# Optimization experiments

Hardware: AMD Instinct MI355X
Metric: run time of the kernel (lower is better)

The kernel has to match this reference:

```python
import jax, jax.numpy as jnp
import numpy as np

LR = 0.001       # ISTA step size (default in _IstaStep)
GAMMA = 0.1      # lambdav sparsity penalty (gamma init kwarg)
N_STEPS = 10     # number of unrolled ISTA iterations


def _soft_threshold(x, t):
    # _proxOp: max(x - t, 0) + min(x + t, 0)
    return jnp.maximum(x - t, 0.0) + jnp.minimum(x + t, 0.0)


def setup_inputs() -> dict:
    key = jax.random.key(0)
    k1, k2 = jax.random.split(key)
    B, I, O = 131072, 128, 256
    inputs = jax.random.normal(k1, (B, I), dtype=jnp.float32)
    # glorot_uniform for W of shape (output_dim, input_dim)
    scale = float(np.sqrt(6.0 / (O + I)))
    W = jax.random.uniform(k2, (O, I), dtype=jnp.float32, minval=-scale, maxval=scale)
    return {"inputs": inputs, "W": W}


def reference(inputs, W):
    # inputs: [B, I]; W: [O, I]; states x: [B, O]
    B = inputs.shape[0]
    O = W.shape[0]
    x0 = jnp.zeros((B, O), dtype=inputs.dtype)

    def step(x, _):
        recon = x @ W                              # [B, I], linear activation
        # analytic grad of sum((inputs - recon)^2) w.r.t. x (what T.grad computes)
        grad = 2.0 * (recon - inputs) @ W.T        # [B, O]
        new_x = _soft_threshold(x - LR * grad, LR * GAMMA)
        # theano.gradient.disconnected_grad on the new state each step
        new_x = jax.lax.stop_gradient(new_x)
        return new_x, None

    x_final, _ = jax.lax.scan(step, x0, None, length=N_STEPS)
    # return_reconstruction=True -> dot(outs, W)
    return x_final @ W
```

## Files before the change

kernel.cpp:

```cpp
#include <hip/hip_runtime.h>
#include <hip/hip_bf16.h>

typedef __attribute__((ext_vector_type(4))) float  f32x4;
typedef __attribute__((ext_vector_type(16))) float f32x16;
typedef __attribute__((ext_vector_type(8))) short  s16x8;
typedef __attribute__((ext_vector_type(4))) short  s16x4;

#define THR_  1.0e-4f
#define SC_   2.0e-3f

__device__ __forceinline__ unsigned short f2bf(float f) {
  union { __hip_bfloat16 b; unsigned short u; } cv;
  cv.b = __float2bfloat16(f);
  return cv.u;
}

__device__ __forceinline__ float sthr(float v) {
  return v - fmaxf(fminf(v, THR_), -THR_);
}

__global__ void sc_prep(const float* __restrict__ W, unsigned short* __restrict__ ws) {
  const int b = blockIdx.x;
  const int l = threadIdx.x;
  const int r = l & 31, h = l >> 5;
  if (b < 128) {
    const int kc = b >> 3, ntg = b & 7;
    const int n = ntg * 32 + r;
    const int k0 = kc * 16 + 8 * h;
    float s[8];
    #pragma unroll
    for (int j = 0; j < 8; ++j) s[j] = 0.0f;
    for (int i = 0; i < 128; ++i) {
      const float wn = W[n * 128 + i];
      #pragma unroll
      for (int j = 0; j < 8; ++j) s[j] += W[(k0 + j) * 128 + i] * wn;
    }
    unsigned short* dst = ws + ((unsigned)b * 64u + l) * 8u;
    #pragma unroll
    for (int j = 0; j < 8; ++j) dst[j] = f2bf(-SC_ * s[j]);
  } else if (b < 192) {
    const int bb = b - 128;
    const int kc = bb >> 3, ntg = bb & 7;
    const int n = ntg * 32 + r;
    const int k0 = kc * 16 + 8 * h;
    unsigned short* dst = ws + 65536u + ((unsigned)bb * 64u + l) * 8u;
    #pragma unroll
    for (int j = 0; j < 8; ++j) dst[j] = f2bf(SC_ * W[n * 128 + k0 + j]);
  } else {
    const int bb = b - 192;
    const int kc = bb >> 2, it = bb & 3;
    const int i = it * 32 + r;
    const int n0 = kc * 16 + 8 * h;
    unsigned short* dst = ws + 98304u + ((unsigned)bb * 64u + l) * 8u;
    #pragma unroll
    for (int j = 0; j < 8; ++j) dst[j] = f2bf(W[(n0 + j) * 128 + i]);
  }
}

__global__ __launch_bounds__(256, 2) void sc_fused(
    const float* __restrict__ inp,
    const unsigned short* __restrict__ wsp,
    float* __restrict__ outp)
{
  __shared__ __align__(16) unsigned char lds[33280];

  const int tid = threadIdx.x;
  const int l = tid & 63;
  const int w = tid >> 6;
  const int h = l >> 5;
  const int r31 = l & 31;
  const long row0 = (long)blockIdx.x * 32;

  const int rB0 = r31 * 520 + h * 16;
  const int rB1 = rB0 + 16640;
  const int wB0 = r31 * 520 + h * 8 + w * 128;
  const int wB1 = wB0 + 16640;

  #pragma unroll
  for (int rep = 0; rep < 4; ++rep) {
    const int flat = rep * 256 + tid;
    const int rr = flat >> 5;
    const int c4 = flat & 31;
    const f32x4 v = *reinterpret_cast<const f32x4*>(inp + (row0 + rr) * 128 + c4 * 4);
    s16x4 p;
    p[0] = (short)f2bf(v[0]); p[1] = (short)f2bf(v[1]);
    p[2] = (short)f2bf(v[2]); p[3] = (short)f2bf(v[3]);
    *reinterpret_cast<s16x4*>(lds + 16640 + rr * 264 + c4 * 8) = p;
  }

  s16x8 gfr[32];
  #pragma unroll
  for (int kc = 0; kc < 8; ++kc)
    #pragma unroll
    for (int nt = 0; nt < 2; ++nt)
      gfr[kc * 2 + nt] = *reinterpret_cast<const s16x8*>(
          wsp + 65536u + ((unsigned)(kc * 8 + w * 2 + nt) * 64u + l) * 8u);

  __syncthreads();

  f32x16 xacc[2], creg[2];
  #pragma unroll
  for (int nt = 0; nt < 2; ++nt)
    #pragma unroll
    for (int e = 0; e < 16; ++e) xacc[nt][e] = 0.0f;

  const int ib = 16640 + r31 * 264 + h * 16;
  #pragma unroll
  for (int kc = 0; kc < 8; ++kc) {
    const s16x8 b = *reinterpret_cast<const s16x8*>(lds + ib + kc * 32);
    __builtin_amdgcn_s_setprio(1);
    #pragma unroll
    for (int nt = 0; nt < 2; ++nt)
      xacc[nt] = __builtin_amdgcn_mfma_f32_32x32x16_bf16(gfr[kc * 2 + nt], b, xacc[nt], 0, 0, 0);
    __builtin_amdgcn_s_setprio(0);
  }

  #pragma unroll
  for (int nt = 0; nt < 2; ++nt) {
    creg[nt] = xacc[nt];
    #pragma unroll
    for (int q = 0; q < 4; ++q) {
      float f0 = sthr(xacc[nt][4 * q + 0]), f1 = sthr(xacc[nt][4 * q + 1]);
      float f2 = sthr(xacc[nt][4 * q + 2]), f3 = sthr(xacc[nt][4 * q + 3]);
      xacc[nt][4 * q + 0] = f0; xacc[nt][4 * q + 1] = f1;
      xacc[nt][4 * q + 2] = f2; xacc[nt][4 * q + 3] = f3;
      s16x4 p;
      p[0] = (short)f2bf(f0); p[1] = (short)f2bf(f1);
      p[2] = (short)f2bf(f2); p[3] = (short)f2bf(f3);
      *reinterpret_cast<s16x4*>(lds + wB0 + nt * 64 + q * 16) = p;
    }
  }

  #pragma unroll
  for (int kc = 0; kc < 16; ++kc)
    #pragma unroll
    for (int nt = 0; nt < 2; ++nt)
      gfr[kc * 2 + nt] = *reinterpret_cast<const s16x8*>(
          wsp + ((unsigned)(kc * 8 + w * 2 + nt) * 64u + l) * 8u);

  auto STEP = [&](const int rb, const int wb) {
    __syncthreads();
    #pragma unroll
    for (int nt = 0; nt < 2; ++nt)
      #pragma unroll
      for (int e = 0; e < 16; ++e) xacc[nt][e] += creg[nt][e];
    #pragma unroll
    for (int kc = 0; kc < 16; ++kc) {
      const s16x8 b = *reinterpret_cast<const s16x8*>(lds + rb + kc * 32);
      __builtin_amdgcn_s_setprio(1);
      #pragma unroll
      for (int nt = 0; nt < 2; ++nt)
        xacc[nt] = __builtin_amdgcn_mfma_f32_32x32x16_bf16(gfr[kc * 2 + nt], b, xacc[nt], 0, 0, 0);
      __builtin_amdgcn_s_setprio(0);
    }
    #pragma unroll
    for (int nt = 0; nt < 2; ++nt)
      #pragma unroll
      for (int q = 0; q < 4; ++q) {
        float f0 = sthr(xacc[nt][4 * q + 0]), f1 = sthr(xacc[nt][4 * q + 1]);
        float f2 = sthr(xacc[nt][4 * q + 2]), f3 = sthr(xacc[nt][4 * q + 3]);
        xacc[nt][4 * q + 0] = f0; xacc[nt][4 * q + 1] = f1;
        xacc[nt][4 * q + 2] = f2; xacc[nt][4 * q + 3] = f3;
        s16x4 p;
        p[0] = (short)f2bf(f0); p[1] = (short)f2bf(f1);
        p[2] = (short)f2bf(f2); p[3] = (short)f2bf(f3);
        *reinterpret_cast<s16x4*>(lds + wb + nt * 64 + q * 16) = p;
      }
  };

  #pragma unroll 1
  for (int p = 0; p < 4; ++p) {
    STEP(rB0, wB1);
    STEP(rB1, wB0);
  }
  STEP(rB0, wB1);

  __syncthreads();
  #pragma unroll
  for (int kc = 0; kc < 16; ++kc)
    gfr[kc] = *reinterpret_cast<const s16x8*>(
        wsp + 98304u + ((unsigned)(kc * 4 + w) * 64u + l) * 8u);
  f32x16 oacc;
  #pragma unroll
  for (int e = 0; e < 16; ++e) oacc[e] = 0.0f;
  #pragma unroll
  for (int kc = 0; kc < 16; ++kc) {
    const s16x8 b = *reinterpret_cast<const s16x8*>(lds + rB1 + kc * 32);
    __builtin_amdgcn_s_setprio(1);
    oacc = __builtin_amdgcn_mfma_f32_32x32x16_bf16(gfr[kc], b, oacc, 0, 0, 0);
    __builtin_amdgcn_s_setprio(0);
  }
  const int ob = r31 * 520 + h * 16 + w * 128;
  #pragma unroll
  for (int q = 0; q < 4; ++q) {
    f32x4 p;
    p[0] = oacc[4 * q + 0]; p[1] = oacc[4 * q + 1];
    p[2] = oacc[4 * q + 2]; p[3] = oacc[4 * q + 3];
    *reinterpret_cast<f32x4*>(lds + ob + q * 32) = p;
  }
  __syncthreads();
  #pragma unroll
  for (int rep = 0; rep < 4; ++rep) {
    const int flat = rep * 256 + tid;
    const int rr = flat >> 5;
    const int c4 = flat & 31;
    const f32x4 v = *reinterpret_cast<const f32x4*>(lds + rr * 520 + c4 * 16);
    *reinterpret_cast<f32x4*>(outp + (row0 + rr) * 128 + c4 * 4) = v;
  }
}

extern "C" void kernel_launch(void* const* d_in, const int* in_sizes, int n_in,
                              void* d_out, int out_size, void* d_ws, size_t ws_size,
                              hipStream_t stream) {
  const float* inp = (const float*)d_in[0];
  const float* W   = (const float*)d_in[1];
  unsigned short* ws = (unsigned short*)d_ws;
  float* outp = (float*)d_out;
  const int B = in_sizes[0] / 128;
  sc_prep<<<256, 64, 0, stream>>>(W, ws);
  sc_fused<<<B / 32, 256, 0, stream>>>(inp, ws, outp);
}
```

Baseline: 184.6 us.

## Split MFMA accumulators into two chains and stagger alternate block groups

```diff
diff --git a/kernel.cpp b/kernel.cpp
--- a/kernel.cpp
+++ b/kernel.cpp
@@ -64,6 +64,11 @@
 {
   __shared__ __align__(16) unsigned char lds[33280];
 
+  if ((blockIdx.x >> 8) & 1) {
+    __builtin_amdgcn_s_sleep(15);
+    __builtin_amdgcn_s_sleep(5);
+  }
+
   const int tid = threadIdx.x;
   const int l = tid & 63;
   const int w = tid >> 6;
@@ -98,38 +103,49 @@
 
   __syncthreads();
 
-  f32x16 xacc[2], creg[2];
+  f32x16 accA[2], accB[2], creg[2];
   #pragma unroll
   for (int nt = 0; nt < 2; ++nt)
     #pragma unroll
-    for (int e = 0; e < 16; ++e) xacc[nt][e] = 0.0f;
+    for (int e = 0; e < 16; ++e) { accA[nt][e] = 0.0f; accB[nt][e] = 0.0f; }
 
   const int ib = 16640 + r31 * 264 + h * 16;
   #pragma unroll
-  for (int kc = 0; kc < 8; ++kc) {
-    const s16x8 b = *reinterpret_cast<const s16x8*>(lds + ib + kc * 32);
+  for (int kc = 0; kc < 4; ++kc) {
+    const s16x8 bA = *reinterpret_cast<const s16x8*>(lds + ib + kc * 32);
+    const s16x8 bB = *reinterpret_cast<const s16x8*>(lds + ib + (kc + 4) * 32);
     __builtin_amdgcn_s_setprio(1);
     #pragma unroll
     for (int nt = 0; nt < 2; ++nt)
-      xacc[nt] = __builtin_amdgcn_mfma_f32_32x32x16_bf16(gfr[kc * 2 + nt], b, xacc[nt], 0, 0, 0);
+      accA[nt] = __builtin_amdgcn_mfma_f32_32x32x16_bf16(gfr[kc * 2 + nt], bA, accA[nt], 0, 0, 0);
+    #pragma unroll
+    for (int nt = 0; nt < 2; ++nt)
+      accB[nt] = __builtin_amdgcn_mfma_f32_32x32x16_bf16(gfr[(kc + 4) * 2 + nt], bB, accB[nt], 0, 0, 0);
     __builtin_amdgcn_s_setprio(0);
   }
 
   #pragma unroll
-  for (int nt = 0; nt < 2; ++nt) {
-    creg[nt] = xacc[nt];
+  for (int nt = 0; nt < 2; ++nt)
     #pragma unroll
     for (int q = 0; q < 4; ++q) {
-      float f0 = sthr(xacc[nt][4 * q + 0]), f1 = sthr(xacc[nt][4 * q + 1]);
-      float f2 = sthr(xacc[nt][4 * q + 2]), f3 = sthr(xacc[nt][4 * q + 3]);
-      xacc[nt][4 * q + 0] = f0; xacc[nt][4 * q + 1] = f1;
-      xacc[nt][4 * q + 2] = f2; xacc[nt][4 * q + 3] = f3;
+      float f0 = accA[nt][4 * q + 0] + accB[nt][4 * q + 0];
+      float f1 = accA[nt][4 * q + 1] + accB[nt][4 * q + 1];
+      float f2 = accA[nt][4 * q + 2] + accB[nt][4 * q + 2];
+      float f3 = accA[nt][4 * q + 3] + accB[nt][4 * q + 3];
+      creg[nt][4 * q + 0] = f0; creg[nt][4 * q + 1] = f1;
+      creg[nt][4 * q + 2] = f2; creg[nt][4 * q + 3] = f3;
+      f0 = sthr(f0); f1 = sthr(f1); f2 = sthr(f2); f3 = sthr(f3);
       s16x4 p;
       p[0] = (short)f2bf(f0); p[1] = (short)f2bf(f1);
       p[2] = (short)f2bf(f2); p[3] = (short)f2bf(f3);
       *reinterpret_cast<s16x4*>(lds + wB0 + nt * 64 + q * 16) = p;
+      accA[nt][4 * q + 0] = f0 + creg[nt][4 * q + 0];
+      accA[nt][4 * q + 1] = f1 + creg[nt][4 * q + 1];
+      accA[nt][4 * q + 2] = f2 + creg[nt][4 * q + 2];
+      accA[nt][4 * q + 3] = f3 + creg[nt][4 * q + 3];
+      accB[nt][4 * q + 0] = 0.0f; accB[nt][4 * q + 1] = 0.0f;
+      accB[nt][4 * q + 2] = 0.0f; accB[nt][4 * q + 3] = 0.0f;
     }
-  }
 
   #pragma unroll
   for (int kc = 0; kc < 16; ++kc)
@@ -141,30 +157,36 @@
   auto STEP = [&](const int rb, const int wb) {
     __syncthreads();
     #pragma unroll
-    for (int nt = 0; nt < 2; ++nt)
-      #pragma unroll
-      for (int e = 0; e < 16; ++e) xacc[nt][e] += creg[nt][e];
-    #pragma unroll
-    for (int kc = 0; kc < 16; ++kc) {
-      const s16x8 b = *reinterpret_cast<const s16x8*>(lds + rb + kc * 32);
+    for (int kc = 0; kc < 8; ++kc) {
+      const s16x8 bA = *reinterpret_cast<const s16x8*>(lds + rb + kc * 32);
+      const s16x8 bB = *reinterpret_cast<const s16x8*>(lds + rb + (kc + 8) * 32);
       __builtin_amdgcn_s_setprio(1);
       #pragma unroll
       for (int nt = 0; nt < 2; ++nt)
-        xacc[nt] = __builtin_amdgcn_mfma_f32_32x32x16_bf16(gfr[kc * 2 + nt], b, xacc[nt], 0, 0, 0);
+        accA[nt] = __builtin_amdgcn_mfma_f32_32x32x16_bf16(gfr[kc * 2 + nt], bA, accA[nt], 0, 0, 0);
+      #pragma unroll
+      for (int nt = 0; nt < 2; ++nt)
+        accB[nt] = __builtin_amdgcn_mfma_f32_32x32x16_bf16(gfr[(kc + 8) * 2 + nt], bB, accB[nt], 0, 0, 0);
       __builtin_amdgcn_s_setprio(0);
     }
     #pragma unroll
     for (int nt = 0; nt < 2; ++nt)
       #pragma unroll
       for (int q = 0; q < 4; ++q) {
-        float f0 = sthr(xacc[nt][4 * q + 0]), f1 = sthr(xacc[nt][4 * q + 1]);
-        float f2 = sthr(xacc[nt][4 * q + 2]), f3 = sthr(xacc[nt][4 * q + 3]);
-        xacc[nt][4 * q + 0] = f0; xacc[nt][4 * q + 1] = f1;
-        xacc[nt][4 * q + 2] = f2; xacc[nt][4 * q + 3] = f3;
+        float f0 = sthr(accA[nt][4 * q + 0] + accB[nt][4 * q + 0]);
+        float f1 = sthr(accA[nt][4 * q + 1] + accB[nt][4 * q + 1]);
+        float f2 = sthr(accA[nt][4 * q + 2] + accB[nt][4 * q + 2]);
+        float f3 = sthr(accA[nt][4 * q + 3] + accB[nt][4 * q + 3]);
         s16x4 p;
         p[0] = (short)f2bf(f0); p[1] = (short)f2bf(f1);
         p[2] = (short)f2bf(f2); p[3] = (short)f2bf(f3);
         *reinterpret_cast<s16x4*>(lds + wb + nt * 64 + q * 16) = p;
+        accA[nt][4 * q + 0] = f0 + creg[nt][4 * q + 0];
+        accA[nt][4 * q + 1] = f1 + creg[nt][4 * q + 1];
+        accA[nt][4 * q + 2] = f2 + creg[nt][4 * q + 2];
+        accA[nt][4 * q + 3] = f3 + creg[nt][4 * q + 3];
+        accB[nt][4 * q + 0] = 0.0f; accB[nt][4 * q + 1] = 0.0f;
+        accB[nt][4 * q + 2] = 0.0f; accB[nt][4 * q + 3] = 0.0f;
       }
   };
 
@@ -180,22 +202,24 @@
   for (int kc = 0; kc < 16; ++kc)
     gfr[kc] = *reinterpret_cast<const s16x8*>(
         wsp + 98304u + ((unsigned)(kc * 4 + w) * 64u + l) * 8u);
-  f32x16 oacc;
-  #pragma unroll
-  for (int e = 0; e < 16; ++e) oacc[e] = 0.0f;
-  #pragma unroll
-  for (int kc = 0; kc < 16; ++kc) {
-    const s16x8 b = *reinterpret_cast<const s16x8*>(lds + rB1 + kc * 32);
+  f32x16 oA, oB;
+  #pragma unroll
+  for (int e = 0; e < 16; ++e) { oA[e] = 0.0f; oB[e] = 0.0f; }
+  #pragma unroll
+  for (int kc = 0; kc < 8; ++kc) {
+    const s16x8 bA = *reinterpret_cast<const s16x8*>(lds + rB1 + kc * 32);
+    const s16x8 bB = *reinterpret_cast<const s16x8*>(lds + rB1 + (kc + 8) * 32);
     __builtin_amdgcn_s_setprio(1);
-    oacc = __builtin_amdgcn_mfma_f32_32x32x16_bf16(gfr[kc], b, oacc, 0, 0, 0);
+    oA = __builtin_amdgcn_mfma_f32_32x32x16_bf16(gfr[kc], bA, oA, 0, 0, 0);
+    oB = __builtin_amdgcn_mfma_f32_32x32x16_bf16(gfr[kc + 8], bB, oB, 0, 0, 0);
     __builtin_amdgcn_s_setprio(0);
   }
   const int ob = r31 * 520 + h * 16 + w * 128;
   #pragma unroll
   for (int q = 0; q < 4; ++q) {
     f32x4 p;
-    p[0] = oacc[4 * q + 0]; p[1] = oacc[4 * q + 1];
-    p[2] = oacc[4 * q + 2]; p[3] = oacc[4 * q + 3];
+    p[0] = oA[4 * q + 0] + oB[4 * q + 0]; p[1] = oA[4 * q + 1] + oB[4 * q + 1];
+    p[2] = oA[4 * q + 2] + oB[4 * q + 2]; p[3] = oA[4 * q + 3] + oB[4 * q + 3];
     *reinterpret_cast<f32x4*>(lds + ob + q * 32) = p;
   }
   __syncthreads();
```

Result: faster. 179.7 us (-2.7%).

## Process two row tiles per block and interleave their ISTA steps

Applied to the files above, without the earlier changes.

```diff
diff --git a/kernel.cpp b/kernel.cpp
--- a/kernel.cpp
+++ b/kernel.cpp
@@ -14,9 +14,14 @@
   cv.b = __float2bfloat16(f);
   return cv.u;
 }
-
 __device__ __forceinline__ float sthr(float v) {
   return v - fmaxf(fminf(v, THR_), -THR_);
+}
+__device__ __forceinline__ float bflo(unsigned u) {
+  return __builtin_bit_cast(float, u << 16);
+}
+__device__ __forceinline__ float bfhi(unsigned u) {
+  return __builtin_bit_cast(float, u & 0xffff0000u);
 }
 
 __global__ void sc_prep(const float* __restrict__ W, unsigned short* __restrict__ ws) {
@@ -62,22 +67,26 @@
     const unsigned short* __restrict__ wsp,
     float* __restrict__ outp)
 {
-  __shared__ __align__(16) unsigned char lds[33280];
+  __shared__ __align__(16) unsigned char lds[66560];
+
+  if ((blockIdx.x >> 8) & 1) {
+    __builtin_amdgcn_s_sleep(15);
+    __builtin_amdgcn_s_sleep(5);
+  }
 
   const int tid = threadIdx.x;
   const int l = tid & 63;
   const int w = tid >> 6;
   const int h = l >> 5;
   const int r31 = l & 31;
-  const long row0 = (long)blockIdx.x * 32;
-
-  const int rB0 = r31 * 520 + h * 16;
-  const int rB1 = rB0 + 16640;
-  const int wB0 = r31 * 520 + h * 8 + w * 128;
-  const int wB1 = wB0 + 16640;
-
-  #pragma unroll
-  for (int rep = 0; rep < 4; ++rep) {
+  const long row0 = (long)blockIdx.x * 64;
+
+  const int rB = r31 * 520 + h * 16;
+  const int wB = r31 * 520 + h * 8 + w * 128;
+  const int ob = r31 * 520 + w * 128 + h * 16;
+
+  #pragma unroll
+  for (int rep = 0; rep < 8; ++rep) {
     const int flat = rep * 256 + tid;
     const int rr = flat >> 5;
     const int c4 = flat & 31;
@@ -85,7 +94,8 @@
     s16x4 p;
     p[0] = (short)f2bf(v[0]); p[1] = (short)f2bf(v[1]);
     p[2] = (short)f2bf(v[2]); p[3] = (short)f2bf(v[3]);
-    *reinterpret_cast<s16x4*>(lds + 16640 + rr * 264 + c4 * 8) = p;
+    const int base = 16640 + (rr >> 5) * 33280 + (rr & 31) * 264;
+    *reinterpret_cast<s16x4*>(lds + base + c4 * 8) = p;
   }
 
   s16x8 gfr[32];
@@ -98,38 +108,51 @@
 
   __syncthreads();
 
-  f32x16 xacc[2], creg[2];
-  #pragma unroll
-  for (int nt = 0; nt < 2; ++nt)
-    #pragma unroll
-    for (int e = 0; e < 16; ++e) xacc[nt][e] = 0.0f;
-
-  const int ib = 16640 + r31 * 264 + h * 16;
+  f32x16 accT[2], accU[2];
+  #pragma unroll
+  for (int nt = 0; nt < 2; ++nt)
+    #pragma unroll
+    for (int e = 0; e < 16; ++e) { accT[nt][e] = 0.0f; accU[nt][e] = 0.0f; }
+
+  const int ibT = 16640 + r31 * 264 + h * 16;
+  const int ibU = ibT + 33280;
   #pragma unroll
   for (int kc = 0; kc < 8; ++kc) {
-    const s16x8 b = *reinterpret_cast<const s16x8*>(lds + ib + kc * 32);
+    const s16x8 bT = *reinterpret_cast<const s16x8*>(lds + ibT + kc * 32);
+    const s16x8 bU = *reinterpret_cast<const s16x8*>(lds + ibU + kc * 32);
     __builtin_amdgcn_s_setprio(1);
-    #pragma unroll
-    for (int nt = 0; nt < 2; ++nt)
-      xacc[nt] = __builtin_amdgcn_mfma_f32_32x32x16_bf16(gfr[kc * 2 + nt], b, xacc[nt], 0, 0, 0);
+    accT[0] = __builtin_amdgcn_mfma_f32_32x32x16_bf16(gfr[kc * 2 + 0], bT, accT[0], 0, 0, 0);
+    accT[1] = __builtin_amdgcn_mfma_f32_32x32x16_bf16(gfr[kc * 2 + 1], bT, accT[1], 0, 0, 0);
+    accU[0] = __builtin_amdgcn_mfma_f32_32x32x16_bf16(gfr[kc * 2 + 0], bU, accU[0], 0, 0, 0);
+    accU[1] = __builtin_amdgcn_mfma_f32_32x32x16_bf16(gfr[kc * 2 + 1], bU, accU[1], 0, 0, 0);
     __builtin_amdgcn_s_setprio(0);
   }
 
-  #pragma unroll
-  for (int nt = 0; nt < 2; ++nt) {
-    creg[nt] = xacc[nt];
+  unsigned cpT[16], cpU[16];
+  #pragma unroll
+  for (int nt = 0; nt < 2; ++nt)
+    #pragma unroll
+    for (int j = 0; j < 8; ++j) {
+      cpT[nt * 8 + j] = (unsigned)f2bf(accT[nt][2 * j]) |
+                        ((unsigned)f2bf(accT[nt][2 * j + 1]) << 16);
+      cpU[nt * 8 + j] = (unsigned)f2bf(accU[nt][2 * j]) |
+                        ((unsigned)f2bf(accU[nt][2 * j + 1]) << 16);
+    }
+
+  #pragma unroll
+  for (int nt = 0; nt < 2; ++nt)
     #pragma unroll
     for (int q = 0; q < 4; ++q) {
-      float f0 = sthr(xacc[nt][4 * q + 0]), f1 = sthr(xacc[nt][4 * q + 1]);
-      float f2 = sthr(xacc[nt][4 * q + 2]), f3 = sthr(xacc[nt][4 * q + 3]);
-      xacc[nt][4 * q + 0] = f0; xacc[nt][4 * q + 1] = f1;
-      xacc[nt][4 * q + 2] = f2; xacc[nt][4 * q + 3] = f3;
+      float x0 = sthr(accT[nt][4 * q + 0]), x1 = sthr(accT[nt][4 * q + 1]);
+      float x2 = sthr(accT[nt][4 * q + 2]), x3 = sthr(accT[nt][4 * q + 3]);
       s16x4 p;
-      p[0] = (short)f2bf(f0); p[1] = (short)f2bf(f1);
-      p[2] = (short)f2bf(f2); p[3] = (short)f2bf(f3);
-      *reinterpret_cast<s16x4*>(lds + wB0 + nt * 64 + q * 16) = p;
-    }
-  }
+      p[0] = (short)f2bf(x0); p[1] = (short)f2bf(x1);
+      p[2] = (short)f2bf(x2); p[3] = (short)f2bf(x3);
+      *reinterpret_cast<s16x4*>(lds + 0 + wB + nt * 64 + q * 16) = p;
+      const unsigned pa = cpT[nt * 8 + q * 2], pb = cpT[nt * 8 + q * 2 + 1];
+      accT[nt][4 * q + 0] = x0 + bflo(pa); accT[nt][4 * q + 1] = x1 + bfhi(pa);
+      accT[nt][4 * q + 2] = x2 + bflo(pb); accT[nt][4 * q + 3] = x3 + bfhi(pb);
+    }
 
   #pragma unroll
   for (int kc = 0; kc < 16; ++kc)
@@ -138,73 +161,101 @@
       gfr[kc * 2 + nt] = *reinterpret_cast<const s16x8*>(
           wsp + ((unsigned)(kc * 8 + w * 2 + nt) * 64u + l) * 8u);
 
-  auto STEP = [&](const int rb, const int wb) {
-    __syncthreads();
-    #pragma unroll
-    for (int nt = 0; nt < 2; ++nt)
-      #pragma unroll
-      for (int e = 0; e < 16; ++e) xacc[nt][e] += creg[nt][e];
+  auto MSTEP = [&](f32x16* acc, const int rbase) {
+    __builtin_amdgcn_s_setprio(1);
     #pragma unroll
     for (int kc = 0; kc < 16; ++kc) {
-      const s16x8 b = *reinterpret_cast<const s16x8*>(lds + rb + kc * 32);
-      __builtin_amdgcn_s_setprio(1);
-      #pragma unroll
-      for (int nt = 0; nt < 2; ++nt)
-        xacc[nt] = __builtin_amdgcn_mfma_f32_32x32x16_bf16(gfr[kc * 2 + nt], b, xacc[nt], 0, 0, 0);
-      __builtin_amdgcn_s_setprio(0);
-    }
+      const s16x8 b = *reinterpret_cast<const s16x8*>(lds + rbase + rB + kc * 32);
+      acc[0] = __builtin_amdgcn_mfma_f32_32x32x16_bf16(gfr[kc * 2 + 0], b, acc[0], 0, 0, 0);
+      acc[1] = __builtin_amdgcn_mfma_f32_32x32x16_bf16(gfr[kc * 2 + 1], b, acc[1], 0, 0, 0);
+    }
+    __builtin_amdgcn_s_setprio(0);
+  };
+  auto WB = [&](f32x16* acc, const unsigned* cp, const int wbase) {
     #pragma unroll
     for (int nt = 0; nt < 2; ++nt)
       #pragma unroll
       for (int q = 0; q < 4; ++q) {
-        float f0 = sthr(xacc[nt][4 * q + 0]), f1 = sthr(xacc[nt][4 * q + 1]);
-        float f2 = sthr(xacc[nt][4 * q + 2]), f3 = sthr(xacc[nt][4 * q + 3]);
-        xacc[nt][4 * q + 0] = f0; xacc[nt][4 * q + 1] = f1;
-        xacc[nt][4 * q + 2] = f2; xacc[nt][4 * q + 3] = f3;
+        float x0 = sthr(acc[nt][4 * q + 0]), x1 = sthr(acc[nt][4 * q + 1]);
+        float x2 = sthr(acc[nt][4 * q + 2]), x3 = sthr(acc[nt][4 * q + 3]);
         s16x4 p;
-        p[0] = (short)f2bf(f0); p[1] = (short)f2bf(f1);
-        p[2] = (short)f2bf(f2); p[3] = (short)f2bf(f3);
-        *reinterpret_cast<s16x4*>(lds + wb + nt * 64 + q * 16) = p;
+        p[0] = (short)f2bf(x0); p[1] = (short)f2bf(x1);
+        p[2] = (short)f2bf(x2); p[3] = (short)f2bf(x3);
+        *reinterpret_cast<s16x4*>(lds + wbase + wB + nt * 64 + q * 16) = p;
+        const unsigned pa = cp[nt * 8 + q * 2], pb = cp[nt * 8 + q * 2 + 1];
+        acc[nt][4 * q + 0] = x0 + bflo(pa); acc[nt][4 * q + 1] = x1 + bfhi(pa);
+        acc[nt][4 * q + 2] = x2 + bflo(pb); acc[nt][4 * q + 3] = x3 + bfhi(pb);
       }
   };
 
+  __syncthreads();
+
   #pragma unroll 1
-  for (int p = 0; p < 4; ++p) {
-    STEP(rB0, wB1);
-    STEP(rB1, wB0);
-  }
-  STEP(rB0, wB1);
-
-  __syncthreads();
+  for (int i = 0; i < 9; ++i) {
+    const int par = i & 1;
+    MSTEP(accT, par ? 16640 : 0);
+    WB(accU, cpU, par ? 49920 : 33280);
+    __syncthreads();
+    MSTEP(accU, par ? 49920 : 33280);
+    WB(accT, cpT, par ? 0 : 16640);
+    __syncthreads();
+  }
+
   #pragma unroll
   for (int kc = 0; kc < 16; ++kc)
     gfr[kc] = *reinterpret_cast<const s16x8*>(
         wsp + 98304u + ((unsigned)(kc * 4 + w) * 64u + l) * 8u);
-  f32x16 oacc;
-  #pragma unroll
-  for (int e = 0; e < 16; ++e) oacc[e] = 0.0f;
+
+  #pragma unroll
+  for (int e = 0; e < 16; ++e) accT[0][e] = 0.0f;
+  __builtin_amdgcn_s_setprio(1);
   #pragma unroll
   for (int kc = 0; kc < 16; ++kc) {
-    const s16x8 b = *reinterpret_cast<const s16x8*>(lds + rB1 + kc * 32);
-    __builtin_amdgcn_s_setprio(1);
-    oacc = __builtin_amdgcn_mfma_f32_32x32x16_bf16(gfr[kc], b, oacc, 0, 0, 0);
-    __builtin_amdgcn_s_setprio(0);
-  }
-  const int ob = r31 * 520 + h * 16 + w * 128;
+    const s16x8 b = *reinterpret_cast<const s16x8*>(lds + 16640 + rB + kc * 32);
+    accT[0] = __builtin_amdgcn_mfma_f32_32x32x16_bf16(gfr[kc], b, accT[0], 0, 0, 0);
+  }
+  __builtin_amdgcn_s_setprio(0);
+  #pragma unroll
+  for (int nt = 0; nt < 2; ++nt)
+    #pragma unroll
+    for (int q = 0; q < 4; ++q) {
+      float x0 = sthr(accU[nt][4 * q + 0]), x1 = sthr(accU[nt][4 * q + 1]);
+      float x2 = sthr(accU[nt][4 * q + 2]), x3 = sthr(accU[nt][4 * q + 3]);
+      s16x4 p;
+      p[0] = (short)f2bf(x0); p[1] = (short)f2bf(x1);
+      p[2] = (short)f2bf(x2); p[3] = (short)f2bf(x3);
+      *reinterpret_cast<s16x4*>(lds + 49920 + wB + nt * 64 + q * 16) = p;
+    }
+  __syncthreads();
+
+  #pragma unroll
+  for (int e = 0; e < 16; ++e) accU[0][e] = 0.0f;
+  __builtin_amdgcn_s_setprio(1);
+  #pragma unroll
+  for (int kc = 0; kc < 16; ++kc) {
+    const s16x8 b = *reinterpret_cast<const s16x8*>(lds + 49920 + rB + kc * 32);
+    accU[0] = __builtin_amdgcn_mfma_f32_32x32x16_bf16(gfr[kc], b, accU[0], 0, 0, 0);
+  }
+  __builtin_amdgcn_s_setprio(0);
   #pragma unroll
   for (int q = 0; q < 4; ++q) {
-    f32x4 p;
-    p[0] = oacc[4 * q + 0]; p[1] = oacc[4 * q + 1];
-    p[2] = oacc[4 * q + 2]; p[3] = oacc[4 * q + 3];
-    *reinterpret_cast<f32x4*>(lds + ob + q * 32) = p;
-  }
-  __syncthreads();
-  #pragma unroll
-  for (int rep = 0; rep < 4; ++rep) {
+    f32x4 pT, pU;
+    pT[0] = accT[0][4 * q + 0]; pT[1] = accT[0][4 * q + 1];
+    pT[2] = accT[0][4 * q + 2]; pT[3] = accT[0][4 * q + 3];
+    pU[0] = accU[0][4 * q + 0]; pU[1] = accU[0][4 * q + 1];
+    pU[2] = accU[0][4 * q + 2]; pU[3] = accU[0][4 * q + 3];
+    *reinterpret_cast<f32x4*>(lds + 0     + ob + q * 32) = pT;
+    *reinterpret_cast<f32x4*>(lds + 33280 + ob + q * 32) = pU;
+  }
+  __syncthreads();
+
+  #pragma unroll
+  for (int rep = 0; rep < 8; ++rep) {
     const int flat = rep * 256 + tid;
     const int rr = flat >> 5;
     const int c4 = flat & 31;
-    const f32x4 v = *reinterpret_cast<const f32x4*>(lds + rr * 520 + c4 * 16);
+    const int base = (rr >> 5) * 33280 + (rr & 31) * 520;
+    const f32x4 v = *reinterpret_cast<const f32x4*>(lds + base + c4 * 16);
     *reinterpret_cast<f32x4*>(outp + (row0 + rr) * 128 + c4 * 4) = v;
   }
 }
@@ -218,5 +269,5 @@
   float* outp = (float*)d_out;
   const int B = in_sizes[0] / 128;
   sc_prep<<<256, 64, 0, stream>>>(W, ws);
-  sc_fused<<<B / 32, 256, 0, stream>>>(inp, ws, outp);
-}
+  sc_fused<<<B / 64, 256, 0, stream>>>(inp, ws, outp);
+}
```

Measured after the change: 234.1 us. 1.27x slower.

## Process 64 rows per block and pack the constant term as bf16

Applied to the files above, without the earlier changes.

```diff
diff --git a/kernel.cpp b/kernel.cpp
--- a/kernel.cpp
+++ b/kernel.cpp
@@ -14,9 +14,14 @@
   cv.b = __float2bfloat16(f);
   return cv.u;
 }
-
 __device__ __forceinline__ float sthr(float v) {
   return v - fmaxf(fminf(v, THR_), -THR_);
+}
+__device__ __forceinline__ float bflo(unsigned u) {
+  return __builtin_bit_cast(float, u << 16);
+}
+__device__ __forceinline__ float bfhi(unsigned u) {
+  return __builtin_bit_cast(float, u & 0xffff0000u);
 }
 
 __global__ void sc_prep(const float* __restrict__ W, unsigned short* __restrict__ ws) {
@@ -62,22 +67,22 @@
     const unsigned short* __restrict__ wsp,
     float* __restrict__ outp)
 {
-  __shared__ __align__(16) unsigned char lds[33280];
+  __shared__ __align__(16) unsigned char lds[66560];
 
   const int tid = threadIdx.x;
   const int l = tid & 63;
   const int w = tid >> 6;
   const int h = l >> 5;
   const int r31 = l & 31;
-  const long row0 = (long)blockIdx.x * 32;
-
-  const int rB0 = r31 * 520 + h * 16;
-  const int rB1 = rB0 + 16640;
-  const int wB0 = r31 * 520 + h * 8 + w * 128;
-  const int wB1 = wB0 + 16640;
-
-  #pragma unroll
-  for (int rep = 0; rep < 4; ++rep) {
+  const long row0 = (long)blockIdx.x * 64;
+
+  const int rBm0 = r31 * 520 + h * 16;
+  const int rBm1 = rBm0 + 32 * 520;
+  const int wBm0 = r31 * 520 + w * 128 + h * 8;
+  const int wBm1 = wBm0 + 32 * 520;
+
+  #pragma unroll
+  for (int rep = 0; rep < 8; ++rep) {
     const int flat = rep * 256 + tid;
     const int rr = flat >> 5;
     const int c4 = flat & 31;
@@ -85,7 +90,7 @@
     s16x4 p;
     p[0] = (short)f2bf(v[0]); p[1] = (short)f2bf(v[1]);
     p[2] = (short)f2bf(v[2]); p[3] = (short)f2bf(v[3]);
-    *reinterpret_cast<s16x4*>(lds + 16640 + rr * 264 + c4 * 8) = p;
+    *reinterpret_cast<s16x4*>(lds + 33280 + rr * 264 + c4 * 8) = p;
   }
 
   s16x8 gfr[32];
@@ -98,38 +103,58 @@
 
   __syncthreads();
 
-  f32x16 xacc[2], creg[2];
+  f32x16 acc[2][2];
   #pragma unroll
   for (int nt = 0; nt < 2; ++nt)
     #pragma unroll
-    for (int e = 0; e < 16; ++e) xacc[nt][e] = 0.0f;
-
-  const int ib = 16640 + r31 * 264 + h * 16;
+    for (int mg = 0; mg < 2; ++mg)
+      #pragma unroll
+      for (int e = 0; e < 16; ++e) acc[nt][mg][e] = 0.0f;
+
+  const int ib0 = 33280 + r31 * 264 + h * 16;
+  const int ib1 = ib0 + 32 * 264;
   #pragma unroll
   for (int kc = 0; kc < 8; ++kc) {
-    const s16x8 b = *reinterpret_cast<const s16x8*>(lds + ib + kc * 32);
+    const s16x8 b0 = *reinterpret_cast<const s16x8*>(lds + ib0 + kc * 32);
+    const s16x8 b1 = *reinterpret_cast<const s16x8*>(lds + ib1 + kc * 32);
     __builtin_amdgcn_s_setprio(1);
     #pragma unroll
-    for (int nt = 0; nt < 2; ++nt)
-      xacc[nt] = __builtin_amdgcn_mfma_f32_32x32x16_bf16(gfr[kc * 2 + nt], b, xacc[nt], 0, 0, 0);
+    for (int nt = 0; nt < 2; ++nt) {
+      acc[nt][0] = __builtin_amdgcn_mfma_f32_32x32x16_bf16(gfr[kc * 2 + nt], b0, acc[nt][0], 0, 0, 0);
+      acc[nt][1] = __builtin_amdgcn_mfma_f32_32x32x16_bf16(gfr[kc * 2 + nt], b1, acc[nt][1], 0, 0, 0);
+    }
     __builtin_amdgcn_s_setprio(0);
   }
 
-  #pragma unroll
-  for (int nt = 0; nt < 2; ++nt) {
-    creg[nt] = xacc[nt];
-    #pragma unroll
-    for (int q = 0; q < 4; ++q) {
-      float f0 = sthr(xacc[nt][4 * q + 0]), f1 = sthr(xacc[nt][4 * q + 1]);
-      float f2 = sthr(xacc[nt][4 * q + 2]), f3 = sthr(xacc[nt][4 * q + 3]);
-      xacc[nt][4 * q + 0] = f0; xacc[nt][4 * q + 1] = f1;
-      xacc[nt][4 * q + 2] = f2; xacc[nt][4 * q + 3] = f3;
-      s16x4 p;
-      p[0] = (short)f2bf(f0); p[1] = (short)f2bf(f1);
-      p[2] = (short)f2bf(f2); p[3] = (short)f2bf(f3);
-      *reinterpret_cast<s16x4*>(lds + wB0 + nt * 64 + q * 16) = p;
-    }
-  }
+  unsigned cp[32];
+  #pragma unroll
+  for (int nt = 0; nt < 2; ++nt)
+    #pragma unroll
+    for (int mg = 0; mg < 2; ++mg)
+      #pragma unroll
+      for (int j = 0; j < 8; ++j)
+        cp[(nt * 2 + mg) * 8 + j] =
+            (unsigned)f2bf(acc[nt][mg][2 * j]) |
+            ((unsigned)f2bf(acc[nt][mg][2 * j + 1]) << 16);
+  #pragma unroll
+  for (int nt = 0; nt < 2; ++nt)
+    #pragma unroll
+    for (int mg = 0; mg < 2; ++mg)
+      #pragma unroll
+      for (int q = 0; q < 4; ++q) {
+        const unsigned pa = cp[(nt * 2 + mg) * 8 + q * 2];
+        const unsigned pb = cp[(nt * 2 + mg) * 8 + q * 2 + 1];
+        float f0 = sthr(acc[nt][mg][4 * q + 0]);
+        float f1 = sthr(acc[nt][mg][4 * q + 1]);
+        float f2 = sthr(acc[nt][mg][4 * q + 2]);
+        float f3 = sthr(acc[nt][mg][4 * q + 3]);
+        s16x4 p;
+        p[0] = (short)f2bf(f0); p[1] = (short)f2bf(f1);
+        p[2] = (short)f2bf(f2); p[3] = (short)f2bf(f3);
+        *reinterpret_cast<s16x4*>(lds + (mg ? wBm1 : wBm0) + nt * 64 + q * 16) = p;
+        acc[nt][mg][4 * q + 0] = f0 + bflo(pa); acc[nt][mg][4 * q + 1] = f1 + bfhi(pa);
+        acc[nt][mg][4 * q + 2] = f2 + bflo(pb); acc[nt][mg][4 * q + 3] = f3 + bfhi(pb);
+      }
 
   #pragma unroll
   for (int kc = 0; kc < 16; ++kc)
@@ -141,66 +166,77 @@
   auto STEP = [&](const int rb, const int wb) {
     __syncthreads();
     #pragma unroll
+    for (int kc = 0; kc < 16; ++kc) {
+      const s16x8 b0 = *reinterpret_cast<const s16x8*>(lds + rb + rBm0 + kc * 32);
+      const s16x8 b1 = *reinterpret_cast<const s16x8*>(lds + rb + rBm1 + kc * 32);
+      __builtin_amdgcn_s_setprio(1);
+      #pragma unroll
+      for (int nt = 0; nt < 2; ++nt) {
+        acc[nt][0] = __builtin_amdgcn_mfma_f32_32x32x16_bf16(gfr[kc * 2 + nt], b0, acc[nt][0], 0, 0, 0);
+        acc[nt][1] = __builtin_amdgcn_mfma_f32_32x32x16_bf16(gfr[kc * 2 + nt], b1, acc[nt][1], 0, 0, 0);
+      }
+      __builtin_amdgcn_s_setprio(0);
+    }
+    #pragma unroll
     for (int nt = 0; nt < 2; ++nt)
       #pragma unroll
-      for (int e = 0; e < 16; ++e) xacc[nt][e] += creg[nt][e];
-    #pragma unroll
-    for (int kc = 0; kc < 16; ++kc) {
-      const s16x8 b = *reinterpret_cast<const s16x8*>(lds + rb + kc * 32);
-      __builtin_amdgcn_s_setprio(1);
-      #pragma unroll
-      for (int nt = 0; nt < 2; ++nt)
-        xacc[nt] = __builtin_amdgcn_mfma_f32_32x32x16_bf16(gfr[kc * 2 + nt], b, xacc[nt], 0, 0, 0);
-      __builtin_amdgcn_s_setprio(0);
-    }
-    #pragma unroll
-    for (int nt = 0; nt < 2; ++nt)
-      #pragma unroll
-      for (int q = 0; q < 4; ++q) {
-        float f0 = sthr(xacc[nt][4 * q + 0]), f1 = sthr(xacc[nt][4 * q + 1]);
-        float f2 = sthr(xacc[nt][4 * q + 2]), f3 = sthr(xacc[nt][4 * q + 3]);
-        xacc[nt][4 * q + 0] = f0; xacc[nt][4 * q + 1] = f1;
-        xacc[nt][4 * q + 2] = f2; xacc[nt][4 * q + 3] = f3;
-        s16x4 p;
-        p[0] = (short)f2bf(f0); p[1] = (short)f2bf(f1);
-        p[2] = (short)f2bf(f2); p[3] = (short)f2bf(f3);
-        *reinterpret_cast<s16x4*>(lds + wb + nt * 64 + q * 16) = p;
-      }
+      for (int mg = 0; mg < 2; ++mg)
+        #pragma unroll
+        for (int q = 0; q < 4; ++q) {
+          const unsigned pa = cp[(nt * 2 + mg) * 8 + q * 2];
+          const unsigned pb = cp[(nt * 2 + mg) * 8 + q * 2 + 1];
+          float f0 = sthr(acc[nt][mg][4 * q + 0]);
+          float f1 = sthr(acc[nt][mg][4 * q + 1]);
+          float f2 = sthr(acc[nt][mg][4 * q + 2]);
+          float f3 = sthr(acc[nt][mg][4 * q + 3]);
+          s16x4 p;
+          p[0] = (short)f2bf(f0); p[1] = (short)f2bf(f1);
+          p[2] = (short)f2bf(f2); p[3] = (short)f2bf(f3);
+          *reinterpret_cast<s16x4*>(lds + wb + (mg ? wBm1 : wBm0) + nt * 64 + q * 16) = p;
+          acc[nt][mg][4 * q + 0] = f0 + bflo(pa); acc[nt][mg][4 * q + 1] = f1 + bfhi(pa);
+          acc[nt][mg][4 * q + 2] = f2 + bflo(pb); acc[nt][mg][4 * q + 3] = f3 + bfhi(pb);
+        }
   };
 
   #pragma unroll 1
   for (int p = 0; p < 4; ++p) {
-    STEP(rB0, wB1);
-    STEP(rB1, wB0);
-  }
-  STEP(rB0, wB1);
+    STEP(0, 33280);
+    STEP(33280, 0);
+  }
+  STEP(0, 33280);
 
   __syncthreads();
   #pragma unroll
   for (int kc = 0; kc < 16; ++kc)
     gfr[kc] = *reinterpret_cast<const s16x8*>(
         wsp + 98304u + ((unsigned)(kc * 4 + w) * 64u + l) * 8u);
-  f32x16 oacc;
-  #pragma unroll
-  for (int e = 0; e < 16; ++e) oacc[e] = 0.0f;
+  f32x16 oacc[2];
+  #pragma unroll
+  for (int mg = 0; mg < 2; ++mg)
+    #pragma unroll
+    for (int e = 0; e < 16; ++e) oacc[mg][e] = 0.0f;
   #pragma unroll
   for (int kc = 0; kc < 16; ++kc) {
-    const s16x8 b = *reinterpret_cast<const s16x8*>(lds + rB1 + kc * 32);
+    const s16x8 b0 = *reinterpret_cast<const s16x8*>(lds + 33280 + rBm0 + kc * 32);
+    const s16x8 b1 = *reinterpret_cast<const s16x8*>(lds + 33280 + rBm1 + kc * 32);
     __builtin_amdgcn_s_setprio(1);
-    oacc = __builtin_amdgcn_mfma_f32_32x32x16_bf16(gfr[kc], b, oacc, 0, 0, 0);
+    oacc[0] = __builtin_amdgcn_mfma_f32_32x32x16_bf16(gfr[kc], b0, oacc[0], 0, 0, 0);
+    oacc[1] = __builtin_amdgcn_mfma_f32_32x32x16_bf16(gfr[kc], b1, oacc[1], 0, 0, 0);
     __builtin_amdgcn_s_setprio(0);
   }
-  const int ob = r31 * 520 + h * 16 + w * 128;
-  #pragma unroll
-  for (int q = 0; q < 4; ++q) {
-    f32x4 p;
-    p[0] = oacc[4 * q + 0]; p[1] = oacc[4 * q + 1];
-    p[2] = oacc[4 * q + 2]; p[3] = oacc[4 * q + 3];
-    *reinterpret_cast<f32x4*>(lds + ob + q * 32) = p;
-  }
+  const int ob0 = r31 * 520 + w * 128 + h * 16;
+  #pragma unroll
+  for (int mg = 0; mg < 2; ++mg)
+    #pragma unroll
+    for (int q = 0; q < 4; ++q) {
+      f32x4 p;
+      p[0] = oacc[mg][4 * q + 0]; p[1] = oacc[mg][4 * q + 1];
+      p[2] = oacc[mg][4 * q + 2]; p[3] = oacc[mg][4 * q + 3];
+      *reinterpret_cast<f32x4*>(lds + ob0 + mg * 16640 + q * 32) = p;
+    }
   __syncthreads();
   #pragma unroll
-  for (int rep = 0; rep < 4; ++rep) {
+  for (int rep = 0; rep < 8; ++rep) {
     const int flat = rep * 256 + tid;
     const int rr = flat >> 5;
     const int c4 = flat & 31;
@@ -218,5 +254,5 @@
   float* outp = (float*)d_out;
   const int B = in_sizes[0] / 128;
   sc_prep<<<256, 64, 0, stream>>>(W, ws);
-  sc_fused<<<B / 32, 256, 0, stream>>>(inp, ws, outp);
-}
+  sc_fused<<<B / 64, 256, 0, stream>>>(inp, ws, outp);
+}
```

Result: slower. 376.8 us (+104.1%).
